# Optimization experiments

Measured on AMD Instinct MI355X. Metric: run time of the kernel, lower is better.

## Reference

```python
import jax, jax.numpy as jnp
import numpy as np

TAU = 2.0
V_TH = 0.5
SG_ALPHA = 4.0
BN_EPS = 1e-5
NUM_HEADS = 8

@jax.custom_vjp
def spike_fn(x):
    return (x >= 0.0).astype(x.dtype)

def _spike_fwd(x):
    return (x >= 0.0).astype(x.dtype), x

def _spike_bwd(x, g):
    s = jax.nn.sigmoid(SG_ALPHA * x)
    return (g * SG_ALPHA * s * (1.0 - s),)

spike_fn.defvjp(_spike_fwd, _spike_bwd)

def lif(x_seq):
    """Multi-step LIF (spikingjelly step_mode='m'): x_seq [T, ...] -> spikes [T, ...].
    v <- v + (x - v)/tau ; spike = H(v - v_th) ; hard reset with detached spike."""
    def step(v, x):
        v = v + (x - v) / TAU
        s = spike_fn(v - V_TH)
        v = v * (1.0 - jax.lax.stop_gradient(s))
        return v, s
    _, s_seq = jax.lax.scan(step, jnp.zeros_like(x_seq[0]), x_seq)
    return s_seq

def conv1x1(x, w, b=None):
    # x: [T,B,C,H,W], w: [Cout,Cin]
    y = jnp.einsum('tbchw,oc->tbohw', x, w)
    if b is not None:
        y = y + b[:, None, None]
    return y

def bn(x, p):
    # eval-mode BatchNorm2d; p = [gamma, beta, mean, var] each [C]
    g, b, m, v = p[0], p[1], p[2], p[3]
    scale = g / jnp.sqrt(v + BN_EPS)
    return x * scale[:, None, None] + (b - m * scale)[:, None, None]

def setup_inputs() -> dict:
    key = jax.random.key(0)
    ks = jax.random.split(key, 20)
    T, B, C, H, W = 4, 8, 512, 32, 32
    Ch = 2048
    def bn_params(k, c):
        kk = jax.random.split(k, 4)
        gamma = jax.random.uniform(kk[0], (c,), jnp.float32, 0.5, 1.5)
        beta = jax.random.normal(kk[1], (c,), jnp.float32) * 0.1
        mean = jax.random.normal(kk[2], (c,), jnp.float32) * 0.1
        var = jax.random.uniform(kk[3], (c,), jnp.float32, 0.5, 1.5)
        return jnp.stack([gamma, beta, mean, var])
    s = 1.0 / np.sqrt(C)
    sh = 1.0 / np.sqrt(Ch)
    return {
        'x': jax.random.normal(ks[0], (T, B, C, H, W), jnp.float32),
        'q_w': jax.random.normal(ks[1], (C, C), jnp.float32) * s,
        'q_bn': bn_params(ks[2], C),
        'k_w': jax.random.normal(ks[3], (C, C), jnp.float32) * s,
        'k_bn': bn_params(ks[4], C),
        'v_w': jax.random.normal(ks[5], (C, C), jnp.float32) * s,
        'v_bn': bn_params(ks[6], C),
        'th_w': jax.random.normal(ks[7], (NUM_HEADS, NUM_HEADS), jnp.float32) / np.sqrt(NUM_HEADS),
        'proj_w': jax.random.normal(ks[8], (C, C), jnp.float32) * s,
        'proj_b': jax.random.normal(ks[9], (C,), jnp.float32) * 0.02,
        'proj_bn': bn_params(ks[10], C),
        'fc1_w': jax.random.normal(ks[11], (Ch, C), jnp.float32) * s,
        'fc1_b': jax.random.normal(ks[12], (Ch,), jnp.float32) * 0.02,
        'fc1_bn': bn_params(ks[13], Ch),
        'fc2_w': jax.random.normal(ks[14], (C, Ch), jnp.float32) * sh,
        'fc2_b': jax.random.normal(ks[15], (C,), jnp.float32) * 0.02,
        'fc2_bn': bn_params(ks[16], C),
    }

def reference(x, q_w, q_bn, k_w, k_bn, v_w, v_bn, th_w, proj_w, proj_b, proj_bn,
              fc1_w, fc1_b, fc1_bn, fc2_w, fc2_b, fc2_bn):
    T, B, C, H, W = x.shape
    N = H * W
    h = NUM_HEADS
    d = C // h

    # ---- MS_SSA_Conv ----
    identity = x
    xs = lif(x)  # shortcut_lif

    def to_heads(t):  # [T,B,C,H,W] -> [T,B,h,N,d]
        t = t.reshape(T, B, C, N).transpose(0, 1, 3, 2)        # [T,B,N,C]
        return t.reshape(T, B, N, h, d).transpose(0, 1, 3, 2, 4)

    q = to_heads(lif(bn(conv1x1(xs, q_w), q_bn)))
    k = to_heads(lif(bn(conv1x1(xs, k_w), k_bn)))
    v = to_heads(lif(bn(conv1x1(xs, v_w), v_bn)))

    kv = (k * v).sum(axis=3, keepdims=True)                    # [T,B,h,1,d]
    kv = jnp.einsum('tbhod,gh->tbgod', kv, th_w)               # talking heads (Conv1d k=1)
    kv = lif(kv)                                               # talking_heads_lif

    x_att = q * kv                                             # [T,B,h,N,d]
    x_att = x_att.transpose(0, 1, 2, 4, 3).reshape(T, B, C, H, W)
    x_out = bn(conv1x1(x_att, proj_w, proj_b), proj_bn) + identity

    # ---- MS_MLP_Conv (res=False since hidden != in) ----
    identity2 = x_out
    hdn = lif(bn(conv1x1(x_out, fc1_w, fc1_b), fc1_bn))
    out = lif(bn(conv1x1(hdn, fc2_w, fc2_b), fc2_bn)) + identity2
    return out
```

## Files before the change

kernel.cpp:

```cpp
#include <hip/hip_runtime.h>

typedef unsigned char u8;
typedef unsigned int u32;

#define T_STEPS 4
#define B_SZ 8
#define C_IN 512
#define CH 2048
#define N_SP 1024
#define S_C ((size_t)B_SZ * C_IN * N_SP)

__global__ __launch_bounds__(256) void lif_x_kernel(const float* __restrict__ in,
                                                    u8* __restrict__ out)
{
    size_t i = (size_t)blockIdx.x * 256 + threadIdx.x;
    float v = 0.0f;
    #pragma unroll
    for (int t = 0; t < T_STEPS; ++t) {
        float x = in[(size_t)t * S_C + i];
        v += (x - v) * 0.5f;
        u8 s = (v >= 0.5f) ? 1 : 0;
        out[(size_t)t * S_C + i] = s;
        v = s ? 0.0f : v;
    }
}

template<int TN, int MODE, int BSRC, bool BIAS, int K, int CO, int NSEL>
__global__ __launch_bounds__(256) void mm(
    const float* __restrict__ W0, const float* __restrict__ W1, const float* __restrict__ W2,
    const void* __restrict__ Xv,
    const float* __restrict__ bn0, const float* __restrict__ bn1, const float* __restrict__ bn2,
    const float* __restrict__ bias,
    const float* __restrict__ kvsf,
    const float* __restrict__ res,
    void* Y0, void* Y1, void* Y2)
{
    constexpr int BM = 64;
    constexpr int BN = 16 * TN;
    constexpr int NB_CO = CO / BM;
    constexpr int NB_N = N_SP / BN;
    constexpr int KT = K / 16;
    constexpr int XSTR = (TN == 8) ? 136 : 72;

    __shared__ float As[16][76];
    __shared__ float Xs[16][XSTR];

    const int bid = blockIdx.x;
    const int nblk = bid % NB_N;
    int slot = bid / NB_N;
    const int cb = slot % NB_CO; slot /= NB_CO;
    const int sel = (NSEL > 1) ? (slot % NSEL) : 0;
    const int b   = (NSEL > 1) ? (slot / NSEL) : slot;

    const float* W   = (NSEL == 1 || sel == 0) ? W0  : (sel == 1 ? W1  : W2);
    const float* bnp = (NSEL == 1 || sel == 0) ? bn0 : (sel == 1 ? bn1 : bn2);
    void* Yv         = (NSEL == 1 || sel == 0) ? Y0  : (sel == 1 ? Y1  : Y2);

    const int coBase = cb * BM;
    const int n0blk = nblk * BN;
    const int tid = threadIdx.x;
    const int tx = tid & 15, ty = tid >> 4;

    const int wr = tid >> 2;
    const int wk4 = (tid & 3) * 4;

    float scale[4], shift[4];
    #pragma unroll
    for (int i = 0; i < 4; ++i) {
        const int co = coBase + ty * 4 + i;
        const float g = bnp[co], be = bnp[CO + co];
        const float mn = bnp[2 * CO + co], vr = bnp[3 * CO + co];
        scale[i] = g / sqrtf(vr + 1e-5f);
        shift[i] = be - mn * scale[i];
        if (BIAS) shift[i] += bias[co] * scale[i];
    }

    float vst[4][TN];
    if (MODE != 1) {
        #pragma unroll
        for (int i = 0; i < 4; ++i)
            #pragma unroll
            for (int j = 0; j < TN; ++j) vst[i][j] = 0.0f;
    }

    for (int t = 0; t < T_STEPS; ++t) {
        const int tb = t * B_SZ + b;
        const u8* Xu = (const u8*)Xv + (size_t)tb * K * N_SP;
        const float* Xf = (const float*)Xv + (size_t)tb * K * N_SP;

        float acc[4][TN];
        #pragma unroll
        for (int i = 0; i < 4; ++i)
            #pragma unroll
            for (int j = 0; j < TN; ++j) acc[i][j] = 0.0f;

        float4 wreg;
        u32 xa = 0, xb = 0;
        float mreg = 1.0f;
        float4 xfa, xfb;

        auto prefetch = [&](int kt) {
            wreg = *reinterpret_cast<const float4*>(
                W + (size_t)(coBase + wr) * K + kt * 16 + wk4);
            if constexpr (BSRC <= 1) {
                const u8* xp = Xu + (size_t)(kt * 16 + ty) * N_SP + n0blk + tx * 4;
                xa = *reinterpret_cast<const u32*>(xp);
                if constexpr (TN == 8)
                    xb = *reinterpret_cast<const u32*>(xp + 64);
                if constexpr (BSRC == 1)
                    mreg = kvsf[(size_t)tb * K + kt * 16 + ty];
            } else {
                const float* xp = Xf + (size_t)(kt * 16 + ty) * N_SP + n0blk + tx * 4;
                xfa = *reinterpret_cast<const float4*>(xp);
                if constexpr (TN == 8)
                    xfb = *reinterpret_cast<const float4*>(xp + 64);
            }
        };

        prefetch(0);

        for (int kt = 0; kt < KT; ++kt) {
            __syncthreads();
            As[wk4 + 0][wr] = wreg.x;
            As[wk4 + 1][wr] = wreg.y;
            As[wk4 + 2][wr] = wreg.z;
            As[wk4 + 3][wr] = wreg.w;
            if constexpr (BSRC <= 1) {
                float4 s0;
                s0.x = (float)( xa        & 0xFFu);
                s0.y = (float)((xa >> 8 ) & 0xFFu);
                s0.z = (float)((xa >> 16) & 0xFFu);
                s0.w = (float)( xa >> 24        );
                if constexpr (BSRC == 1) {
                    s0.x *= mreg; s0.y *= mreg; s0.z *= mreg; s0.w *= mreg;
                }
                *reinterpret_cast<float4*>(&Xs[ty][tx * 4]) = s0;
                if constexpr (TN == 8) {
                    float4 s1;
                    s1.x = (float)( xb        & 0xFFu);
                    s1.y = (float)((xb >> 8 ) & 0xFFu);
                    s1.z = (float)((xb >> 16) & 0xFFu);
                    s1.w = (float)( xb >> 24        );
                    if constexpr (BSRC == 1) {
                        s1.x *= mreg; s1.y *= mreg; s1.z *= mreg; s1.w *= mreg;
                    }
                    *reinterpret_cast<float4*>(&Xs[ty][tx * 4 + 64]) = s1;
                }
            } else {
                *reinterpret_cast<float4*>(&Xs[ty][tx * 4]) = xfa;
                if constexpr (TN == 8)
                    *reinterpret_cast<float4*>(&Xs[ty][tx * 4 + 64]) = xfb;
            }
            __syncthreads();
            if (kt + 1 < KT) prefetch(kt + 1);

            #pragma unroll
            for (int kk = 0; kk < 16; ++kk) {
                float4 av = *reinterpret_cast<const float4*>(&As[kk][ty * 4]);
                float4 x0 = *reinterpret_cast<const float4*>(&Xs[kk][tx * 4]);
                float wa[4] = {av.x, av.y, av.z, av.w};
                float xw[8];
                xw[0] = x0.x; xw[1] = x0.y; xw[2] = x0.z; xw[3] = x0.w;
                if constexpr (TN == 8) {
                    float4 x1 = *reinterpret_cast<const float4*>(&Xs[kk][tx * 4 + 64]);
                    xw[4] = x1.x; xw[5] = x1.y; xw[6] = x1.z; xw[7] = x1.w;
                }
                #pragma unroll
                for (int i = 0; i < 4; ++i)
                    #pragma unroll
                    for (int j = 0; j < TN; ++j)
                        acc[i][j] += wa[i] * xw[j];
            }
        }

        #pragma unroll
        for (int i = 0; i < 4; ++i) {
            const int co = coBase + ty * 4 + i;
            const size_t base = ((size_t)tb * CO + co) * N_SP + n0blk + tx * 4;
            #pragma unroll
            for (int h = 0; h < TN / 4; ++h) {
                const size_t off = base + h * 64;
                if constexpr (MODE == 0) {
                    u32 pk = 0;
                    #pragma unroll
                    for (int e = 0; e < 4; ++e) {
                        const int j = h * 4 + e;
                        const float y = acc[i][j] * scale[i] + shift[i];
                        float v = vst[i][j];
                        v += (y - v) * 0.5f;
                        const u32 s = (v >= 0.5f) ? 1u : 0u;
                        vst[i][j] = s ? 0.0f : v;
                        pk |= s << (8 * e);
                    }
                    *reinterpret_cast<u32*>((u8*)Yv + off) = pk;
                } else if constexpr (MODE == 1) {
                    float4 r0 = *reinterpret_cast<const float4*>(res + off);
                    float rr[4] = {r0.x, r0.y, r0.z, r0.w};
                    float o[4];
                    #pragma unroll
                    for (int e = 0; e < 4; ++e)
                        o[e] = acc[i][h * 4 + e] * scale[i] + shift[i] + rr[e];
                    float4 s0 = {o[0], o[1], o[2], o[3]};
                    *reinterpret_cast<float4*>((float*)Yv + off) = s0;
                } else {
                    float* op = (float*)Yv + off;
                    float4 r0 = *reinterpret_cast<const float4*>(op);
                    float rr[4] = {r0.x, r0.y, r0.z, r0.w};
                    float o[4];
                    #pragma unroll
                    for (int e = 0; e < 4; ++e) {
                        const int j = h * 4 + e;
                        const float y = acc[i][j] * scale[i] + shift[i];
                        float v = vst[i][j];
                        v += (y - v) * 0.5f;
                        const u32 s = (v >= 0.5f) ? 1u : 0u;
                        vst[i][j] = s ? 0.0f : v;
                        o[e] = rr[e] + (s ? 1.0f : 0.0f);
                    }
                    float4 s0 = {o[0], o[1], o[2], o[3]};
                    *reinterpret_cast<float4*>(op) = s0;
                }
            }
        }
    }
}

__global__ __launch_bounds__(256) void kv_reduce(const u8* __restrict__ ks,
                                                 const u8* __restrict__ vs,
                                                 float* __restrict__ kv)
{
    const int row = blockIdx.x * 4 + (threadIdx.x >> 6);
    const int lane = threadIdx.x & 63;
    const u8* kp = ks + (size_t)row * N_SP;
    const u8* vp = vs + (size_t)row * N_SP;
    int acc = 0;
    #pragma unroll
    for (int n = 0; n < N_SP; n += 256) {
        uchar4 a = *reinterpret_cast<const uchar4*>(kp + n + lane * 4);
        uchar4 c = *reinterpret_cast<const uchar4*>(vp + n + lane * 4);
        acc += (a.x & c.x) + (a.y & c.y) + (a.z & c.z) + (a.w & c.w);
    }
    #pragma unroll
    for (int off = 32; off; off >>= 1) acc += __shfl_down(acc, off, 64);
    if (lane == 0) kv[row] = (float)acc;
}

__global__ __launch_bounds__(256) void th_lif(const float* __restrict__ kvraw,
                                              const float* __restrict__ th,
                                              float* __restrict__ kvs)
{
    const int i = blockIdx.x * 256 + threadIdx.x;
    const int b = i >> 9;
    const int c = i & 511;
    const int g = c >> 6;
    const int dd = c & 63;
    float v = 0.0f;
    #pragma unroll
    for (int t = 0; t < T_STEPS; ++t) {
        const float* base = kvraw + ((size_t)t * B_SZ + b) * C_IN;
        float x = 0.0f;
        #pragma unroll
        for (int hh = 0; hh < 8; ++hh)
            x += base[hh * 64 + dd] * th[g * 8 + hh];
        v += (x - v) * 0.5f;
        const float s = (v >= 0.5f) ? 1.0f : 0.0f;
        kvs[((size_t)t * B_SZ + b) * C_IN + c] = s;
        v = (s != 0.0f) ? 0.0f : v;
    }
}

extern "C" void kernel_launch(void* const* d_in, const int* in_sizes, int n_in,
                              void* d_out, int out_size, void* d_ws, size_t ws_size,
                              hipStream_t stream)
{
    const float* x       = (const float*)d_in[0];
    const float* q_w     = (const float*)d_in[1];
    const float* q_bn    = (const float*)d_in[2];
    const float* k_w     = (const float*)d_in[3];
    const float* k_bn    = (const float*)d_in[4];
    const float* v_w     = (const float*)d_in[5];
    const float* v_bn    = (const float*)d_in[6];
    const float* th_w    = (const float*)d_in[7];
    const float* proj_w  = (const float*)d_in[8];
    const float* proj_b  = (const float*)d_in[9];
    const float* proj_bn = (const float*)d_in[10];
    const float* fc1_w   = (const float*)d_in[11];
    const float* fc1_b   = (const float*)d_in[12];
    const float* fc1_bn  = (const float*)d_in[13];
    const float* fc2_w   = (const float*)d_in[14];
    const float* fc2_b   = (const float*)d_in[15];
    const float* fc2_bn  = (const float*)d_in[16];
    float* out = (float*)d_out;

    u8* ws = (u8*)d_ws;
    const size_t SLOT = (size_t)T_STEPS * S_C;
    u8* xs = ws;
    u8* qs = ws + SLOT;
    u8* ks = ws + 2 * SLOT;
    u8* vs = ws + 3 * SLOT;
    float* kvraw = (float*)(ws + 4 * SLOT);
    float* kvsf  = kvraw + (size_t)T_STEPS * B_SZ * C_IN;
    u8* hdn = ws;

    lif_x_kernel<<<(int)(S_C / 256), 256, 0, stream>>>(x, xs);

    mm<8, 0, 0, false, 512, 512, 3><<<1536, 256, 0, stream>>>(
        q_w, k_w, v_w, xs, q_bn, k_bn, v_bn, nullptr, nullptr, nullptr, qs, ks, vs);

    kv_reduce<<<(T_STEPS * B_SZ * C_IN) / 4, 256, 0, stream>>>(ks, vs, kvraw);
    th_lif<<<(B_SZ * C_IN) / 256, 256, 0, stream>>>(kvraw, th_w, kvsf);

    mm<4, 1, 1, true, 512, 512, 1><<<1024, 256, 0, stream>>>(
        proj_w, nullptr, nullptr, qs, proj_bn, nullptr, nullptr, proj_b, kvsf, x,
        out, nullptr, nullptr);

    mm<4, 0, 2, true, 512, 2048, 1><<<4096, 256, 0, stream>>>(
        fc1_w, nullptr, nullptr, out, fc1_bn, nullptr, nullptr, fc1_b, nullptr, nullptr,
        hdn, nullptr, nullptr);

    mm<4, 2, 0, true, 2048, 512, 1><<<1024, 256, 0, stream>>>(
        fc2_w, nullptr, nullptr, hdn, fc2_bn, nullptr, nullptr, fc2_b, nullptr, nullptr,
        out, nullptr, nullptr);
}
```

Before: 2.851 ms.

## Fuse all time steps into one GEMM tile to reuse weight tiles

```diff
diff --git a/kernel.cpp b/kernel.cpp
--- a/kernel.cpp
+++ b/kernel.cpp
@@ -25,7 +25,7 @@
     }
 }
 
-template<int TN, int MODE, int BSRC, bool BIAS, int K, int CO, int NSEL>
+template<int MODE, int BSRC, bool BIAS, int K, int CO, int NSEL>
 __global__ __launch_bounds__(256) void mm(
     const float* __restrict__ W0, const float* __restrict__ W1, const float* __restrict__ W2,
     const void* __restrict__ Xv,
@@ -35,15 +35,12 @@
     const float* __restrict__ res,
     void* Y0, void* Y1, void* Y2)
 {
-    constexpr int BM = 64;
-    constexpr int BN = 16 * TN;
-    constexpr int NB_CO = CO / BM;
-    constexpr int NB_N = N_SP / BN;
+    constexpr int NB_CO = CO / 64;
+    constexpr int NB_N = N_SP / 64;
     constexpr int KT = K / 16;
-    constexpr int XSTR = (TN == 8) ? 136 : 72;
-
-    __shared__ float As[16][76];
-    __shared__ float Xs[16][XSTR];
+
+    __shared__ float As[16][68];
+    __shared__ float Xs[4][16][68];
 
     const int bid = blockIdx.x;
     const int nblk = bid % NB_N;
@@ -56,8 +53,8 @@
     const float* bnp = (NSEL == 1 || sel == 0) ? bn0 : (sel == 1 ? bn1 : bn2);
     void* Yv         = (NSEL == 1 || sel == 0) ? Y0  : (sel == 1 ? Y1  : Y2);
 
-    const int coBase = cb * BM;
-    const int n0blk = nblk * BN;
+    const int coBase = cb * 64;
+    const int n0blk = nblk * 64;
     const int tid = threadIdx.x;
     const int tx = tid & 15, ty = tid >> 4;
 
@@ -75,151 +72,127 @@
         if (BIAS) shift[i] += bias[co] * scale[i];
     }
 
-    float vst[4][TN];
-    if (MODE != 1) {
+    float acc[4][4][4];
+    #pragma unroll
+    for (int t = 0; t < 4; ++t)
         #pragma unroll
         for (int i = 0; i < 4; ++i)
             #pragma unroll
-            for (int j = 0; j < TN; ++j) vst[i][j] = 0.0f;
-    }
-
-    for (int t = 0; t < T_STEPS; ++t) {
-        const int tb = t * B_SZ + b;
-        const u8* Xu = (const u8*)Xv + (size_t)tb * K * N_SP;
-        const float* Xf = (const float*)Xv + (size_t)tb * K * N_SP;
-
-        float acc[4][TN];
-        #pragma unroll
-        for (int i = 0; i < 4; ++i)
-            #pragma unroll
-            for (int j = 0; j < TN; ++j) acc[i][j] = 0.0f;
-
-        float4 wreg;
-        u32 xa = 0, xb = 0;
-        float mreg = 1.0f;
-        float4 xfa, xfb;
-
-        auto prefetch = [&](int kt) {
-            wreg = *reinterpret_cast<const float4*>(
-                W + (size_t)(coBase + wr) * K + kt * 16 + wk4);
+            for (int j = 0; j < 4; ++j) acc[t][i][j] = 0.0f;
+
+    float4 wreg;
+    u32 xu[4];
+    float mreg[4];
+    float4 xf[4];
+
+    auto prefetch = [&](int kt) {
+        wreg = *reinterpret_cast<const float4*>(
+            W + (size_t)(coBase + wr) * K + kt * 16 + wk4);
+        #pragma unroll
+        for (int t = 0; t < 4; ++t) {
+            const int tb = t * B_SZ + b;
             if constexpr (BSRC <= 1) {
-                const u8* xp = Xu + (size_t)(kt * 16 + ty) * N_SP + n0blk + tx * 4;
-                xa = *reinterpret_cast<const u32*>(xp);
-                if constexpr (TN == 8)
-                    xb = *reinterpret_cast<const u32*>(xp + 64);
+                xu[t] = *reinterpret_cast<const u32*>(
+                    (const u8*)Xv + (size_t)tb * K * N_SP
+                    + (size_t)(kt * 16 + ty) * N_SP + n0blk + tx * 4);
                 if constexpr (BSRC == 1)
-                    mreg = kvsf[(size_t)tb * K + kt * 16 + ty];
+                    mreg[t] = kvsf[(size_t)tb * K + kt * 16 + ty];
             } else {
-                const float* xp = Xf + (size_t)(kt * 16 + ty) * N_SP + n0blk + tx * 4;
-                xfa = *reinterpret_cast<const float4*>(xp);
-                if constexpr (TN == 8)
-                    xfb = *reinterpret_cast<const float4*>(xp + 64);
-            }
-        };
-
-        prefetch(0);
-
-        for (int kt = 0; kt < KT; ++kt) {
-            __syncthreads();
-            As[wk4 + 0][wr] = wreg.x;
-            As[wk4 + 1][wr] = wreg.y;
-            As[wk4 + 2][wr] = wreg.z;
-            As[wk4 + 3][wr] = wreg.w;
+                xf[t] = *reinterpret_cast<const float4*>(
+                    (const float*)Xv + (size_t)tb * K * N_SP
+                    + (size_t)(kt * 16 + ty) * N_SP + n0blk + tx * 4);
+            }
+        }
+    };
+
+    prefetch(0);
+
+    for (int kt = 0; kt < KT; ++kt) {
+        __syncthreads();
+        As[wk4 + 0][wr] = wreg.x;
+        As[wk4 + 1][wr] = wreg.y;
+        As[wk4 + 2][wr] = wreg.z;
+        As[wk4 + 3][wr] = wreg.w;
+        #pragma unroll
+        for (int t = 0; t < 4; ++t) {
+            float4 s0;
             if constexpr (BSRC <= 1) {
-                float4 s0;
-                s0.x = (float)( xa        & 0xFFu);
-                s0.y = (float)((xa >> 8 ) & 0xFFu);
-                s0.z = (float)((xa >> 16) & 0xFFu);
-                s0.w = (float)( xa >> 24        );
+                s0.x = (float)( xu[t]        & 0xFFu);
+                s0.y = (float)((xu[t] >> 8 ) & 0xFFu);
+                s0.z = (float)((xu[t] >> 16) & 0xFFu);
+                s0.w = (float)( xu[t] >> 24        );
                 if constexpr (BSRC == 1) {
-                    s0.x *= mreg; s0.y *= mreg; s0.z *= mreg; s0.w *= mreg;
-                }
-                *reinterpret_cast<float4*>(&Xs[ty][tx * 4]) = s0;
-                if constexpr (TN == 8) {
-                    float4 s1;
-                    s1.x = (float)( xb        & 0xFFu);
-                    s1.y = (float)((xb >> 8 ) & 0xFFu);
-                    s1.z = (float)((xb >> 16) & 0xFFu);
-                    s1.w = (float)( xb >> 24        );
-                    if constexpr (BSRC == 1) {
-                        s1.x *= mreg; s1.y *= mreg; s1.z *= mreg; s1.w *= mreg;
-                    }
-                    *reinterpret_cast<float4*>(&Xs[ty][tx * 4 + 64]) = s1;
+                    s0.x *= mreg[t]; s0.y *= mreg[t];
+                    s0.z *= mreg[t]; s0.w *= mreg[t];
                 }
             } else {
-                *reinterpret_cast<float4*>(&Xs[ty][tx * 4]) = xfa;
-                if constexpr (TN == 8)
-                    *reinterpret_cast<float4*>(&Xs[ty][tx * 4 + 64]) = xfb;
-            }
-            __syncthreads();
-            if (kt + 1 < KT) prefetch(kt + 1);
-
+                s0 = xf[t];
+            }
+            *reinterpret_cast<float4*>(&Xs[t][ty][tx * 4]) = s0;
+        }
+        __syncthreads();
+        if (kt + 1 < KT) prefetch(kt + 1);
+
+        #pragma unroll
+        for (int kk = 0; kk < 16; ++kk) {
+            float4 av = *reinterpret_cast<const float4*>(&As[kk][ty * 4]);
+            float wa[4] = {av.x, av.y, av.z, av.w};
             #pragma unroll
-            for (int kk = 0; kk < 16; ++kk) {
-                float4 av = *reinterpret_cast<const float4*>(&As[kk][ty * 4]);
-                float4 x0 = *reinterpret_cast<const float4*>(&Xs[kk][tx * 4]);
-                float wa[4] = {av.x, av.y, av.z, av.w};
-                float xw[8];
-                xw[0] = x0.x; xw[1] = x0.y; xw[2] = x0.z; xw[3] = x0.w;
-                if constexpr (TN == 8) {
-                    float4 x1 = *reinterpret_cast<const float4*>(&Xs[kk][tx * 4 + 64]);
-                    xw[4] = x1.x; xw[5] = x1.y; xw[6] = x1.z; xw[7] = x1.w;
-                }
+            for (int t = 0; t < 4; ++t) {
+                float4 xv = *reinterpret_cast<const float4*>(&Xs[t][kk][tx * 4]);
+                float xw[4] = {xv.x, xv.y, xv.z, xv.w};
                 #pragma unroll
                 for (int i = 0; i < 4; ++i)
                     #pragma unroll
-                    for (int j = 0; j < TN; ++j)
-                        acc[i][j] += wa[i] * xw[j];
-            }
-        }
-
-        #pragma unroll
-        for (int i = 0; i < 4; ++i) {
-            const int co = coBase + ty * 4 + i;
-            const size_t base = ((size_t)tb * CO + co) * N_SP + n0blk + tx * 4;
-            #pragma unroll
-            for (int h = 0; h < TN / 4; ++h) {
-                const size_t off = base + h * 64;
-                if constexpr (MODE == 0) {
-                    u32 pk = 0;
-                    #pragma unroll
-                    for (int e = 0; e < 4; ++e) {
-                        const int j = h * 4 + e;
-                        const float y = acc[i][j] * scale[i] + shift[i];
-                        float v = vst[i][j];
-                        v += (y - v) * 0.5f;
-                        const u32 s = (v >= 0.5f) ? 1u : 0u;
-                        vst[i][j] = s ? 0.0f : v;
-                        pk |= s << (8 * e);
-                    }
-                    *reinterpret_cast<u32*>((u8*)Yv + off) = pk;
-                } else if constexpr (MODE == 1) {
-                    float4 r0 = *reinterpret_cast<const float4*>(res + off);
-                    float rr[4] = {r0.x, r0.y, r0.z, r0.w};
-                    float o[4];
-                    #pragma unroll
-                    for (int e = 0; e < 4; ++e)
-                        o[e] = acc[i][h * 4 + e] * scale[i] + shift[i] + rr[e];
-                    float4 s0 = {o[0], o[1], o[2], o[3]};
-                    *reinterpret_cast<float4*>((float*)Yv + off) = s0;
-                } else {
-                    float* op = (float*)Yv + off;
-                    float4 r0 = *reinterpret_cast<const float4*>(op);
-                    float rr[4] = {r0.x, r0.y, r0.z, r0.w};
-                    float o[4];
-                    #pragma unroll
-                    for (int e = 0; e < 4; ++e) {
-                        const int j = h * 4 + e;
-                        const float y = acc[i][j] * scale[i] + shift[i];
-                        float v = vst[i][j];
-                        v += (y - v) * 0.5f;
-                        const u32 s = (v >= 0.5f) ? 1u : 0u;
-                        vst[i][j] = s ? 0.0f : v;
-                        o[e] = rr[e] + (s ? 1.0f : 0.0f);
-                    }
-                    float4 s0 = {o[0], o[1], o[2], o[3]};
-                    *reinterpret_cast<float4*>(op) = s0;
+                    for (int j = 0; j < 4; ++j)
+                        acc[t][i][j] += wa[i] * xw[j];
+            }
+        }
+    }
+
+    #pragma unroll
+    for (int i = 0; i < 4; ++i) {
+        const int co = coBase + ty * 4 + i;
+        float v[4] = {0.0f, 0.0f, 0.0f, 0.0f};
+        #pragma unroll
+        for (int t = 0; t < 4; ++t) {
+            const int tb = t * B_SZ + b;
+            const size_t off = ((size_t)tb * CO + co) * N_SP + n0blk + tx * 4;
+            if constexpr (MODE == 0) {
+                u32 pk = 0;
+                #pragma unroll
+                for (int e = 0; e < 4; ++e) {
+                    const float y = acc[t][i][e] * scale[i] + shift[i];
+                    v[e] += (y - v[e]) * 0.5f;
+                    const u32 s = (v[e] >= 0.5f) ? 1u : 0u;
+                    v[e] = s ? 0.0f : v[e];
+                    pk |= s << (8 * e);
                 }
+                *reinterpret_cast<u32*>((u8*)Yv + off) = pk;
+            } else if constexpr (MODE == 1) {
+                float4 r0 = *reinterpret_cast<const float4*>(res + off);
+                float rr[4] = {r0.x, r0.y, r0.z, r0.w};
+                float o[4];
+                #pragma unroll
+                for (int e = 0; e < 4; ++e)
+                    o[e] = acc[t][i][e] * scale[i] + shift[i] + rr[e];
+                float4 s0 = {o[0], o[1], o[2], o[3]};
+                *reinterpret_cast<float4*>((float*)Yv + off) = s0;
+            } else {
+                float* op = (float*)Yv + off;
+                float4 r0 = *reinterpret_cast<const float4*>(op);
+                float rr[4] = {r0.x, r0.y, r0.z, r0.w};
+                float o[4];
+                #pragma unroll
+                for (int e = 0; e < 4; ++e) {
+                    const float y = acc[t][i][e] * scale[i] + shift[i];
+                    v[e] += (y - v[e]) * 0.5f;
+                    const u32 s = (v[e] >= 0.5f) ? 1u : 0u;
+                    v[e] = s ? 0.0f : v[e];
+                    o[e] = rr[e] + (s ? 1.0f : 0.0f);
+                }
+                float4 s0 = {o[0], o[1], o[2], o[3]};
+                *reinterpret_cast<float4*>(op) = s0;
             }
         }
     }
@@ -304,21 +277,21 @@
 
     lif_x_kernel<<<(int)(S_C / 256), 256, 0, stream>>>(x, xs);
 
-    mm<8, 0, 0, false, 512, 512, 3><<<1536, 256, 0, stream>>>(
+    mm<0, 0, false, 512, 512, 3><<<3072, 256, 0, stream>>>(
         q_w, k_w, v_w, xs, q_bn, k_bn, v_bn, nullptr, nullptr, nullptr, qs, ks, vs);
 
     kv_reduce<<<(T_STEPS * B_SZ * C_IN) / 4, 256, 0, stream>>>(ks, vs, kvraw);
     th_lif<<<(B_SZ * C_IN) / 256, 256, 0, stream>>>(kvraw, th_w, kvsf);
 
-    mm<4, 1, 1, true, 512, 512, 1><<<1024, 256, 0, stream>>>(
+    mm<1, 1, true, 512, 512, 1><<<1024, 256, 0, stream>>>(
         proj_w, nullptr, nullptr, qs, proj_bn, nullptr, nullptr, proj_b, kvsf, x,
         out, nullptr, nullptr);
 
-    mm<4, 0, 2, true, 512, 2048, 1><<<4096, 256, 0, stream>>>(
+    mm<0, 2, true, 512, 2048, 1><<<4096, 256, 0, stream>>>(
         fc1_w, nullptr, nullptr, out, fc1_bn, nullptr, nullptr, fc1_b, nullptr, nullptr,
         hdn, nullptr, nullptr);
 
-    mm<4, 2, 0, true, 2048, 512, 1><<<1024, 256, 0, stream>>>(
+    mm<2, 0, true, 2048, 512, 1><<<1024, 256, 0, stream>>>(
         fc2_w, nullptr, nullptr, hdn, fc2_bn, nullptr, nullptr, fc2_b, nullptr, nullptr,
         out, nullptr, nullptr);
 }
```

New measurement: 2.390 ms. 1.19x faster.
